# Kernel tuning notes

Measured on AMD Instinct MI355X. Metric: run time of the kernel, lower is better.

## Reference

```python
import jax, jax.numpy as jnp
import numpy as np
import math

B, S, D, H, DH, R = 2, 2048, 1024, 16, 64, 8
EPS = 1e-5


def setup_inputs() -> dict:
    key = jax.random.key(0)
    ks = jax.random.split(key, 8)
    hidden_states = jax.random.normal(ks[0], (B, S, D), jnp.float32)
    # causal boolean mask (batch, seq, seq); every row has >=1 valid entry
    causal = jnp.tril(jnp.ones((S, S), dtype=bool))
    attention_mask = jnp.broadcast_to(causal, (B, S, S))
    # lora: (n_layers=1, 4, batch, hidden, rank); [0]=qA,[1]=kA,[2]=qB,[3]=kB
    lora = jax.random.normal(ks[1], (1, 4, B, D, R), jnp.float32) * 0.02
    ln_w = jnp.ones((D,), jnp.float32)
    Wq = jax.random.normal(ks[2], (D, D), jnp.float32) * 0.02
    Wk = jax.random.normal(ks[3], (D, D), jnp.float32) * 0.02
    Wv = jax.random.normal(ks[4], (D, D), jnp.float32) * 0.02
    Wo = jax.random.normal(ks[5], (D, D), jnp.float32) * 0.02
    return dict(hidden_states=hidden_states, attention_mask=attention_mask,
                lora=lora, ln_w=ln_w, Wq=Wq, Wk=Wk, Wv=Wv, Wo=Wo)


def _rms_ln(x, w):
    # model_center LayerNorm with bias=False == RMS layernorm
    var = jnp.mean(x * x, axis=-1, keepdims=True)
    return x * jax.lax.rsqrt(var + EPS) * w


def _lora_delta(h, A, Bm):
    # h: (b,s,D), A: (b,D,R), Bm: (b,R,D);  h + (h@A)@Bm * 2
    z = jnp.einsum('bsd,bdr->bsr', h, A)
    return h + jnp.einsum('bsr,brd->bsd', z, Bm) * 2


def reference(hidden_states, attention_mask, lora, ln_w, Wq, Wk, Wv, Wo):
    b, s, _ = hidden_states.shape
    x = _rms_ln(hidden_states, ln_w)
    h_q = x @ Wq.T
    h_k = x @ Wk.T
    h_v = x @ Wv.T
    layer = lora[0]  # (4, b, D, R)
    h_q = _lora_delta(h_q, layer[0], jnp.swapaxes(layer[2], 1, 2))
    h_k = _lora_delta(h_k, layer[1], jnp.swapaxes(layer[3], 1, 2))
    q = h_q.reshape(b, s, H, DH)
    k = h_k.reshape(b, s, H, DH)
    v = h_v.reshape(b, s, H, DH)
    score = jnp.einsum('bqhd,bkhd->bhqk', q, k) / math.sqrt(DH)
    m = attention_mask[:, None, :, :]  # (b,1,s,s)
    score = jnp.where(m, score, -jnp.inf)
    p = jax.nn.softmax(score, axis=-1)
    p = jnp.where(m, p, jnp.float32(0))
    out = jnp.einsum('bhqk,bkhd->bqhd', p, v).reshape(b, s, H * DH)
    out = out @ Wo.T
    return hidden_states + out
```

## Files before the change

### kernel.cpp

```cpp
#include <hip/hip_runtime.h>

typedef __bf16 bf16;
typedef __bf16 bf16x4 __attribute__((ext_vector_type(4)));
typedef __bf16 bf16x8 __attribute__((ext_vector_type(8)));
typedef float f32x4 __attribute__((ext_vector_type(4)));

#define DM 1024
#define NROW 4096
#define SEQ 2048
#define HDIM 64
#define NEGBIG -30000.0f

__device__ __forceinline__ void async16(const bf16* g, bf16* l) {
  __builtin_amdgcn_global_load_lds(
      (const __attribute__((address_space(1))) unsigned int*)g,
      (__attribute__((address_space(3))) unsigned int*)l, 16, 0, 0);
}

template <bool F32OUT>
__device__ __forceinline__ void gemm128(const bf16* __restrict__ A,
                                        const bf16* __restrict__ Bw,
                                        bf16* __restrict__ Cb,
                                        float* __restrict__ Cf,
                                        const float* __restrict__ resid,
                                        int m0, int n0) {
  __shared__ __align__(16) bf16 sA[128 * 32];
  __shared__ __align__(16) bf16 sB[128 * 32];
  const int t = threadIdx.x;
  const int lane = t & 63;
  const int w = t >> 6;
  const int wm = (w & 1) * 64;
  const int wn = (w >> 1) * 64;
  const int lr = lane & 15;
  const int kg = lane >> 4;

  f32x4 acc[4][4];
#pragma unroll
  for (int i = 0; i < 4; i++)
#pragma unroll
    for (int j = 0; j < 4; j++)
#pragma unroll
      for (int r = 0; r < 4; r++) acc[i][j][r] = 0.0f;

  const int srow = t >> 2;
  const int scol = (t & 3) * 8;
  const bf16* gA = A + (size_t)(m0 + srow) * DM + scol;
  const bf16* gB = Bw + (size_t)(n0 + srow) * DM + scol;
  bf16* lA = &sA[t * 8];
  bf16* lB = &sB[t * 8];

  for (int k0 = 0; k0 < DM; k0 += 32) {
    async16(gA + k0, lA);
    async16(gA + k0 + 64 * DM, lA + 2048);
    async16(gB + k0, lB);
    async16(gB + k0 + 64 * DM, lB + 2048);
    __syncthreads();
    bf16x8 av[4], bv[4];
#pragma unroll
    for (int mi = 0; mi < 4; mi++)
      av[mi] = *(const bf16x8*)&sA[(wm + mi * 16 + lr) * 32 + kg * 8];
#pragma unroll
    for (int nj = 0; nj < 4; nj++)
      bv[nj] = *(const bf16x8*)&sB[(wn + nj * 16 + lr) * 32 + kg * 8];
#pragma unroll
    for (int mi = 0; mi < 4; mi++)
#pragma unroll
      for (int nj = 0; nj < 4; nj++)
        acc[mi][nj] = __builtin_amdgcn_mfma_f32_16x16x32_bf16(av[mi], bv[nj],
                                                              acc[mi][nj], 0, 0, 0);
    __syncthreads();
  }

#pragma unroll
  for (int mi = 0; mi < 4; mi++) {
#pragma unroll
    for (int r = 0; r < 4; r++) {
      const int grow = m0 + wm + mi * 16 + kg * 4 + r;
      const size_t base = (size_t)grow * DM + n0 + wn + lr;
#pragma unroll
      for (int nj = 0; nj < 4; nj++) {
        float v = acc[mi][nj][r];
        if (F32OUT) {
          Cf[base + nj * 16] = v + resid[base + nj * 16];
        } else {
          Cb[base + nj * 16] = (bf16)v;
        }
      }
    }
  }
}

__global__ __launch_bounds__(256) void k_cast4(const float* __restrict__ a,
                                               const float* __restrict__ b,
                                               const float* __restrict__ c,
                                               const float* __restrict__ e,
                                               bf16* __restrict__ d) {
  const int i = blockIdx.x * 256 + threadIdx.x;
  const int mat = i >> 18;
  const int off = i & 262143;
  const float* s = (mat == 0) ? a : (mat == 1) ? b : (mat == 2) ? c : e;
  const float4 v = ((const float4*)s)[off];
  bf16x4 o;
  o[0] = (bf16)v.x; o[1] = (bf16)v.y; o[2] = (bf16)v.z; o[3] = (bf16)v.w;
  ((bf16x4*)d)[i] = o;
}

__global__ __launch_bounds__(256) void k_rmsnorm(const float* __restrict__ hin,
                                                 const float* __restrict__ wln,
                                                 bf16* __restrict__ xo) {
  const int row = blockIdx.x;
  const int t = threadIdx.x;
  const float4 h4 = ((const float4*)(hin + (size_t)row * DM))[t];
  float ss = h4.x * h4.x + h4.y * h4.y + h4.z * h4.z + h4.w * h4.w;
#pragma unroll
  for (int off = 1; off < 64; off <<= 1) ss += __shfl_xor(ss, off, 64);
  __shared__ float red[4];
  if ((t & 63) == 0) red[t >> 6] = ss;
  __syncthreads();
  ss = red[0] + red[1] + red[2] + red[3];
  const float inv = rsqrtf(ss * (1.0f / DM) + 1e-5f);
  const float4 w4 = ((const float4*)wln)[t];
  bf16x4 o;
  o[0] = (bf16)(h4.x * inv * w4.x);
  o[1] = (bf16)(h4.y * inv * w4.y);
  o[2] = (bf16)(h4.z * inv * w4.z);
  o[3] = (bf16)(h4.w * inv * w4.w);
  *(bf16x4*)&xo[(size_t)row * DM + t * 4] = o;
}

__global__ __launch_bounds__(256) void k_qkv(const bf16* __restrict__ x,
                                             const bf16* __restrict__ Wq,
                                             const bf16* __restrict__ Wk,
                                             const bf16* __restrict__ Wv,
                                             bf16* __restrict__ hq,
                                             bf16* __restrict__ hk,
                                             bf16* __restrict__ hv) {
  const int nb = blockIdx.y;
  const int wsel = nb >> 3;
  const int n0 = (nb & 7) * 128;
  const bf16* Bw = (wsel == 0) ? Wq : (wsel == 1) ? Wk : Wv;
  bf16* C = (wsel == 0) ? hq : (wsel == 1) ? hk : hv;
  gemm128<false>(x, Bw, C, nullptr, nullptr, blockIdx.x * 128, n0);
}

__global__ __launch_bounds__(256) void k_oproj(const bf16* __restrict__ ctx,
                                               const bf16* __restrict__ Wo,
                                               const float* __restrict__ resid,
                                               float* __restrict__ out) {
  gemm128<true>(ctx, Wo, nullptr, out, resid, blockIdx.x * 128, blockIdx.y * 128);
}

__global__ __launch_bounds__(256) void k_lora2(bf16* __restrict__ hq,
                                               bf16* __restrict__ hk,
                                               const float* __restrict__ lora) {
  const int row0 = blockIdx.x * 32;
  const int which = blockIdx.y;
  const int b = row0 >> 11;
  bf16* H = (which == 0 ? hq : hk) + (size_t)row0 * DM;
  const float* Am = lora + (size_t)(which == 0 ? 0 : 1) * 16384 + (size_t)b * 8192;
  const float* Bm = lora + (size_t)(which == 0 ? 2 : 3) * 16384 + (size_t)b * 8192;
  const int t = threadIdx.x;
  const int lane = t & 63;
  const int w = t >> 6;
  const int lr = lane & 15;
  const int kg = lane >> 4;

  __shared__ __align__(16) bf16 At[8 * 1024];
  __shared__ float Zp[2][32][8];

  const int d0 = lane * 16;
  float4 Bv[32];
  {
    const float4* bp = (const float4*)(Bm + (size_t)d0 * 8);
#pragma unroll
    for (int i = 0; i < 32; i++) Bv[i] = bp[i];
  }

  {
    const float4* ap = (const float4*)(Am + (size_t)t * 32);
#pragma unroll
    for (int i = 0; i < 8; i++) {
      const float4 v = ap[i];
      const int idx = t * 32 + i * 4;
      At[(idx & 7) * 1024 + (idx >> 3)]             = (bf16)v.x;
      At[((idx + 1) & 7) * 1024 + ((idx + 1) >> 3)] = (bf16)v.y;
      At[((idx + 2) & 7) * 1024 + ((idx + 2) >> 3)] = (bf16)v.z;
      At[((idx + 3) & 7) * 1024 + ((idx + 3) >> 3)] = (bf16)v.w;
    }
  }
  __syncthreads();

  const int tile = w & 1;
  const int khalf = w >> 1;
  {
    f32x4 zacc;
#pragma unroll
    for (int r = 0; r < 4; r++) zacc[r] = 0.f;
    const bf16* gH = H + (size_t)(tile * 16 + lr) * DM + khalf * 512 + kg * 8;
    const bf16* lA = &At[(lr & 7) * 1024 + khalf * 512 + kg * 8];
#pragma unroll
    for (int i = 0; i < 16; i++) {
      const bf16x8 ah = *(const bf16x8*)(gH + i * 32);
      const bf16x8 ba = *(const bf16x8*)(lA + i * 32);
      zacc = __builtin_amdgcn_mfma_f32_16x16x32_bf16(ah, ba, zacc, 0, 0, 0);
    }
    if (lr < 8) {
#pragma unroll
      for (int r = 0; r < 4; r++) Zp[khalf][tile * 16 + kg * 4 + r][lr] = zacc[r];
    }
  }
  __syncthreads();

#pragma unroll
  for (int rr = 0; rr < 8; rr++) {
    const int row = w * 8 + rr;
    const float4 z0 = *(const float4*)&Zp[0][row][0];
    const float4 z1 = *(const float4*)&Zp[0][row][4];
    const float4 y0 = *(const float4*)&Zp[1][row][0];
    const float4 y1 = *(const float4*)&Zp[1][row][4];
    const float za = z0.x + y0.x, zb = z0.y + y0.y, zc = z0.z + y0.z, zd = z0.w + y0.w;
    const float ze = z1.x + y1.x, zf = z1.y + y1.y, zg = z1.z + y1.z, zh = z1.w + y1.w;
    bf16* hp = H + (size_t)row * DM + d0;
    const bf16x8 h0 = *(const bf16x8*)hp;
    const bf16x8 h1 = *(const bf16x8*)(hp + 8);
    bf16x8 o0, o1;
#pragma unroll
    for (int j = 0; j < 16; j++) {
      const float4 b0 = Bv[2 * j];
      const float4 b1 = Bv[2 * j + 1];
      const float delta = za * b0.x + zb * b0.y + zc * b0.z + zd * b0.w +
                          ze * b1.x + zf * b1.y + zg * b1.z + zh * b1.w;
      const float hj = (j < 8) ? (float)h0[j] : (float)h1[j - 8];
      const bf16 ov = (bf16)(hj + 2.0f * delta);
      if (j < 8) o0[j] = ov; else o1[j - 8] = ov;
    }
    *(bf16x8*)hp = o0;
    *(bf16x8*)(hp + 8) = o1;
  }
}

#define PAD 72
__global__ __launch_bounds__(256, 4) void k_attn(const bf16* __restrict__ hq,
                                                 const bf16* __restrict__ hk,
                                                 const bf16* __restrict__ hv,
                                                 bf16* __restrict__ ctx) {
  const int n = blockIdx.x;
  const int slab = n & 31;
  const int hh = slab & 15;
  const int b = slab >> 4;
  const int xx = n >> 5;
  const int s = xx >> 3;
  const int v = xx & 7;
  const int qt = (s == 0) ? 4 * v : (s == 1) ? 31 - 4 * v
               : (s == 2) ? 4 * v + 2 : 29 - 4 * v;
  const int qbase = qt * 64;

  const int t = threadIdx.x;
  const int lane = t & 63;
  const int w = t >> 6;
  const int lr = lane & 15;
  const int kg = lane >> 4;

  __shared__ __align__(16) bf16 sQ[64 * PAD];
  __shared__ __align__(16) bf16 sK[64 * PAD];
  __shared__ __align__(16) bf16 sVt[64 * PAD];
  __shared__ __align__(16) bf16 sP[64 * PAD];

  const size_t rowbase = (size_t)b * SEQ;
  const int hoff = hh * HDIM;
  const float sscale = 0.18033688011112042f;

  {
    const int r = t >> 2;
    const int c0 = (t & 3) * 16;
    const bf16* g = hq + (rowbase + qbase + r) * DM + hoff + c0;
    bf16x8 q0 = *(const bf16x8*)g;
    bf16x8 q1 = *(const bf16x8*)(g + 8);
    bf16x8 o0, o1;
#pragma unroll
    for (int j = 0; j < 8; j++) {
      o0[j] = (bf16)((float)q0[j] * sscale);
      o1[j] = (bf16)((float)q1[j] * sscale);
    }
    *(bf16x8*)&sQ[r * PAD + c0] = o0;
    *(bf16x8*)&sQ[r * PAD + c0 + 8] = o1;
  }

  const int rK = t >> 2;
  const int cK = (t & 3) * 16;
  const bf16* gK = hk + (rowbase + rK) * DM + hoff + cK;
  const bf16* gV = hv + (rowbase + lane) * DM + hoff + w * 16;
  bf16x8 kr0 = *(const bf16x8*)gK;
  bf16x8 kr1 = *(const bf16x8*)(gK + 8);
  bf16x8 vr0 = *(const bf16x8*)gV;
  bf16x8 vr1 = *(const bf16x8*)(gV + 8);

  float m_l = NEGBIG, l_l = 0.f;
  f32x4 oacc[4];
#pragma unroll
  for (int nj = 0; nj < 4; nj++)
#pragma unroll
    for (int r = 0; r < 4; r++) oacc[nj][r] = 0.f;

  __syncthreads();

  for (int kt = 0; kt <= qt; kt++) {
    *(bf16x8*)&sK[rK * PAD + cK] = kr0;
    *(bf16x8*)&sK[rK * PAD + cK + 8] = kr1;
    {
      const int c0 = w * 16;
#pragma unroll
      for (int j = 0; j < 8; j++) {
        sVt[(c0 + j) * PAD + lane] = vr0[j];
        sVt[(c0 + 8 + j) * PAD + lane] = vr1[j];
      }
    }
    __syncthreads();

    if (kt < qt) {
      const bf16* gK2 = gK + (size_t)(kt + 1) * 64 * DM;
      const bf16* gV2 = gV + (size_t)(kt + 1) * 64 * DM;
      kr0 = *(const bf16x8*)gK2;
      kr1 = *(const bf16x8*)(gK2 + 8);
      vr0 = *(const bf16x8*)gV2;
      vr1 = *(const bf16x8*)(gV2 + 8);
    }

    f32x4 sc[4];
#pragma unroll
    for (int nj = 0; nj < 4; nj++)
#pragma unroll
      for (int r = 0; r < 4; r++) sc[nj][r] = 0.f;
#pragma unroll
    for (int ks = 0; ks < 2; ks++) {
      const bf16x8 bq = *(const bf16x8*)&sQ[(w * 16 + lr) * PAD + ks * 32 + kg * 8];
#pragma unroll
      for (int nj = 0; nj < 4; nj++) {
        const bf16x8 ak = *(const bf16x8*)&sK[(nj * 16 + lr) * PAD + ks * 32 + kg * 8];
        sc[nj] = __builtin_amdgcn_mfma_f32_16x16x32_bf16(ak, bq, sc[nj], 0, 0, 0);
      }
    }

    if (kt == qt) {
      const int ql = w * 16 + lr;
#pragma unroll
      for (int nj = 0; nj < 4; nj++)
#pragma unroll
        for (int r = 0; r < 4; r++) {
          const int kl = nj * 16 + kg * 4 + r;
          sc[nj][r] = (kl <= ql) ? sc[nj][r] : NEGBIG;
        }
    }

    float rm = sc[0][0];
#pragma unroll
    for (int nj = 0; nj < 4; nj++)
#pragma unroll
      for (int r = 0; r < 4; r++) rm = fmaxf(rm, sc[nj][r]);
    rm = fmaxf(rm, __shfl_xor(rm, 16, 64));
    rm = fmaxf(rm, __shfl_xor(rm, 32, 64));
    const float mnew = fmaxf(m_l, rm);
    const float alpha = __builtin_amdgcn_exp2f(m_l - mnew);
    float rs = 0.f;
#pragma unroll
    for (int nj = 0; nj < 4; nj++)
#pragma unroll
      for (int r = 0; r < 4; r++) {
        const float p = __builtin_amdgcn_exp2f(sc[nj][r] - mnew);
        sc[nj][r] = p;
        rs += p;
      }
    rs += __shfl_xor(rs, 16, 64);
    rs += __shfl_xor(rs, 32, 64);
    l_l = l_l * alpha + rs;
    m_l = mnew;

#pragma unroll
    for (int nj = 0; nj < 4; nj++)
#pragma unroll
      for (int r = 0; r < 4; r++)
        sP[(w * 16 + lr) * PAD + nj * 16 + kg * 4 + r] = (bf16)sc[nj][r];

#pragma unroll
    for (int r = 0; r < 4; r++) {
      const float ar = __shfl(alpha, (lane & 48) | (kg * 4 + r), 64);
#pragma unroll
      for (int nj = 0; nj < 4; nj++) oacc[nj][r] *= ar;
    }

#pragma unroll
    for (int ks = 0; ks < 2; ks++) {
      const bf16x8 ap = *(const bf16x8*)&sP[(w * 16 + lr) * PAD + ks * 32 + kg * 8];
#pragma unroll
      for (int nj = 0; nj < 4; nj++) {
        const bf16x8 bv = *(const bf16x8*)&sVt[(nj * 16 + lr) * PAD + ks * 32 + kg * 8];
        oacc[nj] = __builtin_amdgcn_mfma_f32_16x16x32_bf16(ap, bv, oacc[nj], 0, 0, 0);
      }
    }
    __syncthreads();
  }

#pragma unroll
  for (int r = 0; r < 4; r++) {
    const float lrow = __shfl(l_l, (lane & 48) | (kg * 4 + r), 64);
    const float invl = 1.0f / lrow;
    const int qr = qbase + w * 16 + kg * 4 + r;
    const size_t base = (rowbase + qr) * DM + hoff + lr;
#pragma unroll
    for (int nj = 0; nj < 4; nj++)
      ctx[base + nj * 16] = (bf16)(oacc[nj][r] * invl);
  }
}

extern "C" void kernel_launch(void* const* d_in, const int* in_sizes, int n_in,
                              void* d_out, int out_size, void* d_ws, size_t ws_size,
                              hipStream_t stream) {
  const float* hidden = (const float*)d_in[0];
  const float* lora = (const float*)d_in[2];
  const float* wln  = (const float*)d_in[3];
  const float* Wq   = (const float*)d_in[4];
  const float* Wk   = (const float*)d_in[5];
  const float* Wv   = (const float*)d_in[6];
  const float* Wo   = (const float*)d_in[7];
  float* out = (float*)d_out;

  const size_t BUF = (size_t)NROW * DM;
  if (ws_size < 4 * BUF * sizeof(bf16)) return;
  bf16* ws = (bf16*)d_ws;
  bf16* hq  = ws;
  bf16* hk  = ws + 1 * BUF;
  bf16* hv  = ws + 2 * BUF;
  bf16* ctx = ws + 3 * BUF;

  bf16* dob = (bf16*)d_out;
  bf16* x   = dob;
  bf16* wqb = dob + BUF;
  bf16* wkb = dob + BUF + DM * DM;
  bf16* wvb = dob + BUF + 2 * DM * DM;
  bf16* wob = dob + BUF + 3 * DM * DM;

  k_cast4<<<dim3(4 * 1024), dim3(256), 0, stream>>>(Wq, Wk, Wv, Wo, wqb);
  k_rmsnorm<<<dim3(NROW), dim3(256), 0, stream>>>(hidden, wln, x);
  k_qkv<<<dim3(32, 24), dim3(256), 0, stream>>>(x, wqb, wkb, wvb, hq, hk, hv);
  k_lora2<<<dim3(128, 2), dim3(256), 0, stream>>>(hq, hk, lora);
  k_attn<<<dim3(1024), dim3(256), 0, stream>>>(hq, hk, hv, ctx);
  k_oproj<<<dim3(32, 8), dim3(256), 0, stream>>>(ctx, wob, hidden, out);
}
```

Before: 227.1 us.

## Pre-transpose V globally and use XOR-swizzled LDS tiles in attention

Adds a kernel that transposes V into a head-major (b,h,dh,seq) buffer, reusing the x region of the output buffer after the QKV GEMM has consumed it. The attention kernel can then store V tiles to LDS with vector writes instead of scalar transposing stores. It also replaces padded LDS rows with an XOR swizzle to avoid bank conflicts, and packs P stores into 4-wide vector writes. The cost is an extra launch plus an additional read and write of V through global memory.

```diff
diff --git a/kernel.cpp b/kernel.cpp
--- a/kernel.cpp
+++ b/kernel.cpp
@@ -10,6 +10,9 @@
 #define SEQ 2048
 #define HDIM 64
 #define NEGBIG -30000.0f
+
+#define SWB(base, row, bcol) \
+  ((char*)(base) + (row) * 128 + ((bcol) ^ (((row) & 7) << 4)))
 
 __device__ __forceinline__ void async16(const bf16* g, bf16* l) {
   __builtin_amdgcn_global_load_lds(
@@ -150,6 +153,32 @@
   gemm128<true>(ctx, Wo, nullptr, out, resid, blockIdx.x * 128, blockIdx.y * 128);
 }
 
+__global__ __launch_bounds__(256) void k_vt(const bf16* __restrict__ hv,
+                                            bf16* __restrict__ hvT) {
+  __shared__ __align__(16) bf16 sT[64 * 64];
+  const int t = threadIdx.x;
+  const int s0 = blockIdx.x * 64;
+  const int c0 = blockIdx.y * 64;
+  const int b = blockIdx.z;
+  const int r = t >> 2;
+  const int cc = (t & 3) * 16;
+  const bf16* g = hv + ((size_t)(b * SEQ + s0 + r)) * DM + c0 + cc;
+  const bf16x8 a0 = *(const bf16x8*)g;
+  const bf16x8 a1 = *(const bf16x8*)(g + 8);
+  *(bf16x8*)SWB(sT, r, cc * 2) = a0;
+  *(bf16x8*)SWB(sT, r, cc * 2 + 16) = a1;
+  __syncthreads();
+  bf16x8 o0, o1;
+#pragma unroll
+  for (int j = 0; j < 8; j++) {
+    o0[j] = *(const bf16*)SWB(sT, cc + j, r * 2);
+    o1[j] = *(const bf16*)SWB(sT, cc + 8 + j, r * 2);
+  }
+  bf16* o = hvT + ((size_t)(b * DM + c0 + r)) * SEQ + s0 + cc;
+  *(bf16x8*)o = o0;
+  *(bf16x8*)(o + 8) = o1;
+}
+
 __global__ __launch_bounds__(256) void k_lora2(bf16* __restrict__ hq,
                                                bf16* __restrict__ hk,
                                                const float* __restrict__ lora) {
@@ -239,10 +268,9 @@
   }
 }
 
-#define PAD 72
 __global__ __launch_bounds__(256, 4) void k_attn(const bf16* __restrict__ hq,
                                                  const bf16* __restrict__ hk,
-                                                 const bf16* __restrict__ hv,
+                                                 const bf16* __restrict__ hvT,
                                                  bf16* __restrict__ ctx) {
   const int n = blockIdx.x;
   const int slab = n & 31;
@@ -261,19 +289,21 @@
   const int lr = lane & 15;
   const int kg = lane >> 4;
 
-  __shared__ __align__(16) bf16 sQ[64 * PAD];
-  __shared__ __align__(16) bf16 sK[64 * PAD];
-  __shared__ __align__(16) bf16 sVt[64 * PAD];
-  __shared__ __align__(16) bf16 sP[64 * PAD];
+  __shared__ __align__(16) bf16 sQ[64 * 64];
+  __shared__ __align__(16) bf16 sK[64 * 64];
+  __shared__ __align__(16) bf16 sVt[64 * 64];
+  __shared__ __align__(16) bf16 sP[64 * 64];
 
   const size_t rowbase = (size_t)b * SEQ;
   const int hoff = hh * HDIM;
   const float sscale = 0.18033688011112042f;
 
+  const int r4 = t >> 2;
+  const int ce = (t & 3) * 16;
+  const int cb = (t & 3) * 32;
+
   {
-    const int r = t >> 2;
-    const int c0 = (t & 3) * 16;
-    const bf16* g = hq + (rowbase + qbase + r) * DM + hoff + c0;
+    const bf16* g = hq + (rowbase + qbase + r4) * DM + hoff + ce;
     bf16x8 q0 = *(const bf16x8*)g;
     bf16x8 q1 = *(const bf16x8*)(g + 8);
     bf16x8 o0, o1;
@@ -282,14 +312,12 @@
       o0[j] = (bf16)((float)q0[j] * sscale);
       o1[j] = (bf16)((float)q1[j] * sscale);
     }
-    *(bf16x8*)&sQ[r * PAD + c0] = o0;
-    *(bf16x8*)&sQ[r * PAD + c0 + 8] = o1;
-  }
-
-  const int rK = t >> 2;
-  const int cK = (t & 3) * 16;
-  const bf16* gK = hk + (rowbase + rK) * DM + hoff + cK;
-  const bf16* gV = hv + (rowbase + lane) * DM + hoff + w * 16;
+    *(bf16x8*)SWB(sQ, r4, cb) = o0;
+    *(bf16x8*)SWB(sQ, r4, cb + 16) = o1;
+  }
+
+  const bf16* gK = hk + (rowbase + r4) * DM + hoff + ce;
+  const bf16* gV = hvT + ((size_t)slab * HDIM + r4) * SEQ + ce;
   bf16x8 kr0 = *(const bf16x8*)gK;
   bf16x8 kr1 = *(const bf16x8*)(gK + 8);
   bf16x8 vr0 = *(const bf16x8*)gV;
@@ -305,21 +333,15 @@
   __syncthreads();
 
   for (int kt = 0; kt <= qt; kt++) {
-    *(bf16x8*)&sK[rK * PAD + cK] = kr0;
-    *(bf16x8*)&sK[rK * PAD + cK + 8] = kr1;
-    {
-      const int c0 = w * 16;
-#pragma unroll
-      for (int j = 0; j < 8; j++) {
-        sVt[(c0 + j) * PAD + lane] = vr0[j];
-        sVt[(c0 + 8 + j) * PAD + lane] = vr1[j];
-      }
-    }
+    *(bf16x8*)SWB(sK, r4, cb) = kr0;
+    *(bf16x8*)SWB(sK, r4, cb + 16) = kr1;
+    *(bf16x8*)SWB(sVt, r4, cb) = vr0;
+    *(bf16x8*)SWB(sVt, r4, cb + 16) = vr1;
     __syncthreads();
 
     if (kt < qt) {
       const bf16* gK2 = gK + (size_t)(kt + 1) * 64 * DM;
-      const bf16* gV2 = gV + (size_t)(kt + 1) * 64 * DM;
+      const bf16* gV2 = gV + (kt + 1) * 64;
       kr0 = *(const bf16x8*)gK2;
       kr1 = *(const bf16x8*)(gK2 + 8);
       vr0 = *(const bf16x8*)gV2;
@@ -333,10 +355,10 @@
       for (int r = 0; r < 4; r++) sc[nj][r] = 0.f;
 #pragma unroll
     for (int ks = 0; ks < 2; ks++) {
-      const bf16x8 bq = *(const bf16x8*)&sQ[(w * 16 + lr) * PAD + ks * 32 + kg * 8];
+      const bf16x8 bq = *(const bf16x8*)SWB(sQ, w * 16 + lr, ks * 64 + kg * 16);
 #pragma unroll
       for (int nj = 0; nj < 4; nj++) {
-        const bf16x8 ak = *(const bf16x8*)&sK[(nj * 16 + lr) * PAD + ks * 32 + kg * 8];
+        const bf16x8 ak = *(const bf16x8*)SWB(sK, nj * 16 + lr, ks * 64 + kg * 16);
         sc[nj] = __builtin_amdgcn_mfma_f32_16x16x32_bf16(ak, bq, sc[nj], 0, 0, 0);
       }
     }
@@ -376,10 +398,12 @@
     m_l = mnew;
 
 #pragma unroll
-    for (int nj = 0; nj < 4; nj++)
-#pragma unroll
-      for (int r = 0; r < 4; r++)
-        sP[(w * 16 + lr) * PAD + nj * 16 + kg * 4 + r] = (bf16)sc[nj][r];
+    for (int nj = 0; nj < 4; nj++) {
+      bf16x4 p4;
+#pragma unroll
+      for (int r = 0; r < 4; r++) p4[r] = (bf16)sc[nj][r];
+      *(bf16x4*)SWB(sP, w * 16 + lr, nj * 32 + kg * 8) = p4;
+    }
 
 #pragma unroll
     for (int r = 0; r < 4; r++) {
@@ -390,10 +414,10 @@
 
 #pragma unroll
     for (int ks = 0; ks < 2; ks++) {
-      const bf16x8 ap = *(const bf16x8*)&sP[(w * 16 + lr) * PAD + ks * 32 + kg * 8];
+      const bf16x8 ap = *(const bf16x8*)SWB(sP, w * 16 + lr, ks * 64 + kg * 16);
 #pragma unroll
       for (int nj = 0; nj < 4; nj++) {
-        const bf16x8 bv = *(const bf16x8*)&sVt[(nj * 16 + lr) * PAD + ks * 32 + kg * 8];
+        const bf16x8 bv = *(const bf16x8*)SWB(sVt, nj * 16 + lr, ks * 64 + kg * 16);
         oacc[nj] = __builtin_amdgcn_mfma_f32_16x16x32_bf16(ap, bv, oacc[nj], 0, 0, 0);
       }
     }
@@ -438,11 +462,13 @@
   bf16* wkb = dob + BUF + DM * DM;
   bf16* wvb = dob + BUF + 2 * DM * DM;
   bf16* wob = dob + BUF + 3 * DM * DM;
+  bf16* hvT = dob;
 
   k_cast4<<<dim3(4 * 1024), dim3(256), 0, stream>>>(Wq, Wk, Wv, Wo, wqb);
   k_rmsnorm<<<dim3(NROW), dim3(256), 0, stream>>>(hidden, wln, x);
   k_qkv<<<dim3(32, 24), dim3(256), 0, stream>>>(x, wqb, wkb, wvb, hq, hk, hv);
+  k_vt<<<dim3(SEQ / 64, DM / 64, 2), dim3(256), 0, stream>>>(hv, hvT);
   k_lora2<<<dim3(128, 2), dim3(256), 0, stream>>>(hq, hk, lora);
-  k_attn<<<dim3(1024), dim3(256), 0, stream>>>(hq, hk, hv, ctx);
+  k_attn<<<dim3(1024), dim3(256), 0, stream>>>(hq, hk, hvT, ctx);
   k_oproj<<<dim3(32, 8), dim3(256), 0, stream>>>(ctx, wob, hidden, out);
 }
```

Result: faster. 222.0 us (-2.3%).
